# Optimization experiments

Hardware: AMD Instinct MI355X
Metric: run time of the kernel (lower is better)

The kernel has to match this reference:

```python
import jax, jax.numpy as jnp
import numpy as np

N, E, H, D, IN = 50000, 800000, 4, 16, 64  # nodes, edges, heads, head dim, in_feats
HD = H * D


def setup_inputs() -> dict:
    key = jax.random.key(0)
    ks = jax.random.split(key, 12)
    inp = {
        "q_src": jax.random.normal(ks[0], (N, H, D), jnp.float32),
        "v_src": jax.random.normal(ks[1], (N, H, D), jnp.float32),
        "feat": jax.random.normal(ks[2], (N, IN), jnp.float32),
        "src": jax.random.randint(ks[3], (E,), 0, N, jnp.int32),
        "dst": jax.random.randint(ks[4], (E,), 0, N, jnp.int32),
        # parameters (torch nn.Linear stores W as [out, in]; we use [in, out])
        "Wk": jax.random.normal(ks[5], (IN, HD), jnp.float32) / np.sqrt(IN),
        "bk": jnp.zeros((HD,), jnp.float32),
        "Wskip": jax.random.normal(ks[6], (IN, HD), jnp.float32) / np.sqrt(IN),
        "bskip": jnp.zeros((HD,), jnp.float32),
        "Wgate": jax.random.normal(ks[7], (3 * HD, 1), jnp.float32) / np.sqrt(3 * HD),
        "bgate": jnp.zeros((1,), jnp.float32),
        "ln_gamma": jnp.ones((HD,), jnp.float32),
        "ln_beta": jnp.zeros((HD,), jnp.float32),
        "prelu_a": jnp.array(0.25, jnp.float32),  # nn.PReLU() default
    }
    return inp


def reference(q_src, v_src, feat, src, dst, Wk, bk, Wskip, bskip, Wgate, bgate, ln_gamma, ln_beta, prelu_a):
    n = feat.shape[0]
    # k_dst = lin_key(h_dst).view(-1, H, D)
    k_dst = (feat @ Wk + bk).reshape(n, H, D)
    # per-edge dot-product scores: u_dot_v('ft','ft') -> [E, H, 1], scaled
    a = jnp.sum(q_src[src] * k_dst[dst], axis=-1, keepdims=True) / np.sqrt(D)
    # edge softmax over incoming edges of each dst node (segment softmax)
    amax = jax.lax.stop_gradient(jax.ops.segment_max(a, dst, num_segments=n))  # [n,H,1]
    ex = jnp.exp(a - amax[dst])
    denom = jax.ops.segment_sum(ex, dst, num_segments=n)  # [n,H,1]
    sa = ex / denom[dst]  # [E,H,1]
    # u_mul_e + sum: weighted scatter-sum aggregation
    agg = jax.ops.segment_sum(v_src[src] * sa, dst, num_segments=n)  # [n,H,D]
    rst = agg.reshape(n, HD)
    # skip connection + gate
    skip = feat @ Wskip + bskip  # [n, HD]
    gate = jax.nn.sigmoid(jnp.concatenate([skip, rst, skip - rst], axis=-1) @ Wgate + bgate)
    rst = gate * skip + (1.0 - gate) * rst
    # LayerNorm over last dim (eps=1e-5)
    mu = jnp.mean(rst, axis=-1, keepdims=True)
    var = jnp.mean(jnp.square(rst - mu), axis=-1, keepdims=True)
    rst = (rst - mu) * jax.lax.rsqrt(var + 1e-5) * ln_gamma + ln_beta
    # PReLU activation
    rst = jnp.where(rst >= 0, rst, prelu_a * rst)
    return rst
```

## Files before the change

kernel.cpp:

```cpp
#include <hip/hip_runtime.h>
#include <hip/hip_fp16.h>

#define NN 50000
#define EE 800000
#define MAXDEG 64
#define NBUCK 98
#define BSHIFT 9
#define BMASK 511
#define CAP 9216
#define AB_BLOCKS 1564

typedef _Float16 f16x8 __attribute__((ext_vector_type(8)));
typedef float    f32x4 __attribute__((ext_vector_type(4)));

union F4H { float4 f4; __half2 h2[4]; };

__global__ void zero_kernel(int* __restrict__ gcursor)
{
    if (threadIdx.x < NBUCK) gcursor[threadIdx.x] = 0;
}

__global__ __launch_bounds__(256) void binpack_kernel(
    const float* __restrict__ feat,
    const float* __restrict__ Wk, const float* __restrict__ bk,
    const float* __restrict__ Ws, const float* __restrict__ bs,
    const float* __restrict__ q, const float* __restrict__ v,
    const int* __restrict__ src, const int* __restrict__ dst,
    __half2* __restrict__ ks,
    __half2* __restrict__ qv, int* __restrict__ gcursor,
    int* __restrict__ staging)
{
    __shared__ f16x8 sFrag[16 * 64];
    __shared__ int hist[NBUCK], gbase[NBUCK];

    int tid = threadIdx.x, bid = blockIdx.x;

    if ((bid & 1) == 0) {
        if (tid < NBUCK) hist[tid] = 0;
        __syncthreads();

        int ebid  = bid >> 1;
        int ebase = ebid * 1024 + tid * 4;
        int4 es, ed;
        int b0 = 0, b1 = 0, b2 = 0, b3 = 0, r0 = 0, r1 = 0, r2 = 0, r3 = 0;
        bool ev = ebase < EE;
        if (ev) {
            es = *(const int4*)(src + ebase);
            ed = *(const int4*)(dst + ebase);
            b0 = ed.x >> BSHIFT; r0 = atomicAdd(&hist[b0], 1);
            b1 = ed.y >> BSHIFT; r1 = atomicAdd(&hist[b1], 1);
            b2 = ed.z >> BSHIFT; r2 = atomicAdd(&hist[b2], 1);
            b3 = ed.w >> BSHIFT; r3 = atomicAdd(&hist[b3], 1);
        }
        __syncthreads();
        if (tid < NBUCK) {
            int h = hist[tid];
            gbase[tid] = h ? atomicAdd(gcursor + tid, h) : 0;
        }
        __syncthreads();
        if (ev) {
            int i0 = gbase[b0] + r0; if (i0 < CAP) staging[b0 * CAP + i0] = (es.x << BSHIFT) | (ed.x & BMASK);
            int i1 = gbase[b1] + r1; if (i1 < CAP) staging[b1 * CAP + i1] = (es.y << BSHIFT) | (ed.y & BMASK);
            int i2 = gbase[b2] + r2; if (i2 < CAP) staging[b2 * CAP + i2] = (es.z << BSHIFT) | (ed.z & BMASK);
            int i3 = gbase[b3] + r3; if (i3 < CAP) staging[b3 * CAP + i3] = (es.w << BSHIFT) | (ed.w & BMASK);
        }
        return;
    }

    int nbid = bid >> 1;
    int wave = tid >> 6, lane = tid & 63;

    for (int i = tid; i < 4096; i += 256) {
        int k = i >> 6, nk = i & 63;
        int kt = k >> 5, j = k & 7;
        int lf = ((k >> 3) & 3) * 16 + (nk & 15);
        ((_Float16*)&sFrag[((nk >> 4) * 2 + kt) * 64 + lf])[j]       = (_Float16)Wk[i];
        ((_Float16*)&sFrag[((4 + (nk >> 4)) * 2 + kt) * 64 + lf])[j] = (_Float16)Ws[i];
    }
    __syncthreads();

    int base16 = nbid * 64 + wave * 16;
    if (base16 < NN) {
        int m  = lane & 15;
        int kg = lane >> 4;
        const float* arow = feat + (size_t)(base16 + m) * 64 + kg * 8;
        float4 fa0 = *(const float4*)(arow + 0);
        float4 fa1 = *(const float4*)(arow + 4);
        float4 fa2 = *(const float4*)(arow + 32);
        float4 fa3 = *(const float4*)(arow + 36);
        f16x8 a0 = { (_Float16)fa0.x,(_Float16)fa0.y,(_Float16)fa0.z,(_Float16)fa0.w,
                     (_Float16)fa1.x,(_Float16)fa1.y,(_Float16)fa1.z,(_Float16)fa1.w };
        f16x8 a1 = { (_Float16)fa2.x,(_Float16)fa2.y,(_Float16)fa2.z,(_Float16)fa2.w,
                     (_Float16)fa3.x,(_Float16)fa3.y,(_Float16)fa3.z,(_Float16)fa3.w };

        f32x4 acc0={0,0,0,0}, acc1={0,0,0,0}, acc2={0,0,0,0}, acc3={0,0,0,0};
        f32x4 acc4={0,0,0,0}, acc5={0,0,0,0}, acc6={0,0,0,0}, acc7={0,0,0,0};

#define COLT(c, ACC) { \
        f16x8 b0 = sFrag[((c)*2 + 0) * 64 + lane]; \
        f16x8 b1 = sFrag[((c)*2 + 1) * 64 + lane]; \
        ACC = __builtin_amdgcn_mfma_f32_16x16x32_f16(a0, b0, ACC, 0, 0, 0); \
        ACC = __builtin_amdgcn_mfma_f32_16x16x32_f16(a1, b1, ACC, 0, 0, 0); }
        COLT(0, acc0) COLT(1, acc1) COLT(2, acc2) COLT(3, acc3)
        COLT(4, acc4) COLT(5, acc5) COLT(6, acc6) COLT(7, acc7)
#undef COLT

        int rbase = base16 + kg * 4;

#define STOREP(COFF, AK, AS) { \
        int col = (COFF) + m; float bbk = bk[col], bbs = bs[col]; \
        ks[(size_t)(rbase + 0) * 64 + col] = __floats2half2_rn(AK[0] + bbk, AS[0] + bbs); \
        ks[(size_t)(rbase + 1) * 64 + col] = __floats2half2_rn(AK[1] + bbk, AS[1] + bbs); \
        ks[(size_t)(rbase + 2) * 64 + col] = __floats2half2_rn(AK[2] + bbk, AS[2] + bbs); \
        ks[(size_t)(rbase + 3) * 64 + col] = __floats2half2_rn(AK[3] + bbk, AS[3] + bbs); }
        STOREP( 0, acc0, acc4) STOREP(16, acc1, acc5)
        STOREP(32, acc2, acc6) STOREP(48, acc3, acc7)
#undef STOREP
    }

    {
        size_t g0 = (size_t)nbid * 4096 + (size_t)tid * 16;
        if ((int)(g0 >> 6) < NN) {
            const float4* qp = (const float4*)(q + g0);
            const float4* vp = (const float4*)(v + g0);
            #pragma unroll
            for (int gI = 0; gI < 4; ++gI) {
                float4 qq = qp[gI], vv = vp[gI];
                F4H outw;
                outw.h2[0] = __floats2half2_rn(qq.x, vv.x);
                outw.h2[1] = __floats2half2_rn(qq.y, vv.y);
                outw.h2[2] = __floats2half2_rn(qq.z, vv.z);
                outw.h2[3] = __floats2half2_rn(qq.w, vv.w);
                *(float4*)(qv + g0 + gI * 4) = outw.f4;
            }
        }
    }
}

__global__ __launch_bounds__(256) void scatter_kernel(
    const int* __restrict__ staging, const int* __restrict__ gcursor,
    unsigned short* __restrict__ sorted_src,
    int* __restrict__ cntA, int* __restrict__ cntB)
{
    __shared__ int cnt[512];
    int b = blockIdx.x >> 1, half = blockIdx.x & 1, tid = threadIdx.x;
    cnt[tid] = 0; cnt[tid + 256] = 0;
    __syncthreads();

    int nE = gcursor[b];
    if (nE > CAP) nE = CAP;
    int lo = half ? (nE >> 1) : 0;
    int hi = half ? nE : (nE >> 1);

    if (half == 0) {
        for (int i = lo + tid; i < hi; i += 256) {
            int e  = staging[b * CAP + i];
            int dl = e & BMASK;
            int pos = atomicAdd(&cnt[dl], 1);
            if (pos < MAXDEG)
                sorted_src[(size_t)((b << BSHIFT) + dl) * MAXDEG + pos] =
                    (unsigned short)(e >> BSHIFT);
        }
    } else {
        for (int i = lo + tid; i < hi; i += 256) {
            int e  = staging[b * CAP + i];
            int dl = e & BMASK;
            int pos = atomicAdd(&cnt[dl], 1);
            int sl = MAXDEG - 1 - pos;
            if (sl >= 0)
                sorted_src[(size_t)((b << BSHIFT) + dl) * MAXDEG + sl] =
                    (unsigned short)(e >> BSHIFT);
        }
    }
    __syncthreads();

    int* cp = half ? cntB : cntA;
    int d0 = (b << BSHIFT) + tid;
    if (d0 < NN) cp[d0] = cnt[tid];
    int d1 = d0 + 256;
    if (d1 < NN) cp[d1] = cnt[tid + 256];
}

__global__ __launch_bounds__(256) void gather_finalize_kernel(
    const __half2* __restrict__ qv,
    const __half2* __restrict__ ks,
    const unsigned short* __restrict__ sorted_src,
    const int*     __restrict__ cntA,
    const int*     __restrict__ cntB,
    const float*   __restrict__ Wg,
    const float*   __restrict__ bg,
    const float*   __restrict__ gamma,
    const float*   __restrict__ beta,
    const float*   __restrict__ prelu_a,
    float* __restrict__ out, int n)
{
    int node = (blockIdx.x * 256 + threadIdx.x) >> 6;
    int lane = threadIdx.x & 63;
    if (node >= n) return;
    int g = lane >> 4;
    int w = lane & 15;
    int slot = w * 4;

    int cA = cntA[node];
    int dcount = cA + cntB[node];
    if (dcount > MAXDEG) dcount = MAXDEG;
    int sidx = (lane < cA) ? lane : (MAXDEG - 1 - (lane - cA));
    int s_all = (lane < dcount) ? (int)sorted_src[(size_t)node * MAXDEG + sidx] : 0;

    F4H ksr;
    ksr.f4 = *(const float4*)(ks + (size_t)node * 64 + slot);
    float2 ks0 = __half22float2(ksr.h2[0]);
    float2 ks1 = __half22float2(ksr.h2[1]);
    float2 ks2 = __half22float2(ksr.h2[2]);
    float2 ks3 = __half22float2(ksr.h2[3]);
    float4 k4;  k4.x = ks0.x;  k4.y = ks1.x;  k4.z = ks2.x;  k4.w = ks3.x;
    float4 sk4; sk4.x = ks0.y; sk4.y = ks1.y; sk4.z = ks2.y; sk4.w = ks3.y;

    float wg0a = Wg[slot],      wg1a = Wg[slot+1],      wg2a = Wg[slot+2],      wg3a = Wg[slot+3];
    float wg0b = Wg[64+slot],   wg1b = Wg[64+slot+1],   wg2b = Wg[64+slot+2],   wg3b = Wg[64+slot+3];
    float wg0c = Wg[128+slot],  wg1c = Wg[128+slot+1],  wg2c = Wg[128+slot+2],  wg3c = Wg[128+slot+3];
    float gm0 = gamma[slot], gm1 = gamma[slot+1], gm2 = gamma[slot+2], gm3 = gamma[slot+3];
    float bt0 = beta[slot],  bt1 = beta[slot+1],  bt2 = beta[slot+2],  bt3 = beta[slot+3];
    float bgv = bg[0];
    float al  = prelu_a[0];

    float den = 0.f;
    float acc0 = 0.f, acc1 = 0.f, acc2 = 0.f, acc3 = 0.f;

    int niter = (dcount + 7) >> 3;
    if (niter > 0) {
        int sA = __shfl(s_all, g);
        int sB = __shfl(s_all, 4 + g);
        F4H rA, rB;
        rA.f4 = *(const float4*)(qv + (size_t)sA * 64 + slot);
        rB.f4 = *(const float4*)(qv + (size_t)sB * 64 + slot);

        for (int it = 0; it < niter; ++it) {
            F4H cAx = rA, cBx = rB;
            int e0 = it * 8;
            if (it + 1 < niter) {
                int sA2 = __shfl(s_all, (e0 + 8 + g) & 63);
                int sB2 = __shfl(s_all, (e0 + 12 + g) & 63);
                rA.f4 = *(const float4*)(qv + (size_t)sA2 * 64 + slot);
                rB.f4 = *(const float4*)(qv + (size_t)sB2 * 64 + slot);
            }

            {
                float2 a0 = __half22float2(cAx.h2[0]);
                float2 a1 = __half22float2(cAx.h2[1]);
                float2 a2 = __half22float2(cAx.h2[2]);
                float2 a3 = __half22float2(cAx.h2[3]);
                float p = a0.x * k4.x + a1.x * k4.y + a2.x * k4.z + a3.x * k4.w;
                p += __shfl_xor(p, 1);
                p += __shfl_xor(p, 2);
                float ex = ((e0 + g) < dcount) ? __expf(p * 0.25f) : 0.f;
                den += ex;
                acc0 = fmaf(ex, a0.y, acc0);
                acc1 = fmaf(ex, a1.y, acc1);
                acc2 = fmaf(ex, a2.y, acc2);
                acc3 = fmaf(ex, a3.y, acc3);
            }

            if (e0 + 4 < dcount) {
                float2 b0 = __half22float2(cBx.h2[0]);
                float2 b1 = __half22float2(cBx.h2[1]);
                float2 b2 = __half22float2(cBx.h2[2]);
                float2 b3 = __half22float2(cBx.h2[3]);
                float p = b0.x * k4.x + b1.x * k4.y + b2.x * k4.z + b3.x * k4.w;
                p += __shfl_xor(p, 1);
                p += __shfl_xor(p, 2);
                float ex = ((e0 + 4 + g) < dcount) ? __expf(p * 0.25f) : 0.f;
                den += ex;
                acc0 = fmaf(ex, b0.y, acc0);
                acc1 = fmaf(ex, b1.y, acc1);
                acc2 = fmaf(ex, b2.y, acc2);
                acc3 = fmaf(ex, b3.y, acc3);
            }
        }
    }

    den  += __shfl_xor(den, 16);  den  += __shfl_xor(den, 32);
    acc0 += __shfl_xor(acc0, 16); acc0 += __shfl_xor(acc0, 32);
    acc1 += __shfl_xor(acc1, 16); acc1 += __shfl_xor(acc1, 32);
    acc2 += __shfl_xor(acc2, 16); acc2 += __shfl_xor(acc2, 32);
    acc3 += __shfl_xor(acc3, 16); acc3 += __shfl_xor(acc3, 32);

    float inv = (den > 0.f) ? 1.f / den : 0.f;
    float r0 = acc0 * inv, r1 = acc1 * inv, r2 = acc2 * inv, r3 = acc3 * inv;

    float gp = sk4.x * wg0a + r0 * wg0b + (sk4.x - r0) * wg0c
             + sk4.y * wg1a + r1 * wg1b + (sk4.y - r1) * wg1c
             + sk4.z * wg2a + r2 * wg2b + (sk4.z - r2) * wg2c
             + sk4.w * wg3a + r3 * wg3b + (sk4.w - r3) * wg3c;
    gp += __shfl_xor(gp, 1);
    gp += __shfl_xor(gp, 2);
    gp += __shfl_xor(gp, 4);
    gp += __shfl_xor(gp, 8);
    float gate = 1.f / (1.f + __expf(-(gp + bgv)));

    float m0 = gate * sk4.x + (1.f - gate) * r0;
    float m1 = gate * sk4.y + (1.f - gate) * r1;
    float m2 = gate * sk4.z + (1.f - gate) * r2;
    float m3 = gate * sk4.w + (1.f - gate) * r3;

    float mu = m0 + m1 + m2 + m3;
    mu += __shfl_xor(mu, 1); mu += __shfl_xor(mu, 2);
    mu += __shfl_xor(mu, 4); mu += __shfl_xor(mu, 8);
    mu *= (1.f / 64.f);
    float d0 = m0 - mu, d1 = m1 - mu, d2 = m2 - mu, d3 = m3 - mu;
    float var = d0 * d0 + d1 * d1 + d2 * d2 + d3 * d3;
    var += __shfl_xor(var, 1); var += __shfl_xor(var, 2);
    var += __shfl_xor(var, 4); var += __shfl_xor(var, 8);
    var *= (1.f / 64.f);
    float rs = rsqrtf(var + 1e-5f);

    float y0 = d0 * rs * gm0 + bt0;
    float y1 = d1 * rs * gm1 + bt1;
    float y2 = d2 * rs * gm2 + bt2;
    float y3 = d3 * rs * gm3 + bt3;
    y0 = (y0 >= 0.f) ? y0 : al * y0;
    y1 = (y1 >= 0.f) ? y1 : al * y1;
    y2 = (y2 >= 0.f) ? y2 : al * y2;
    y3 = (y3 >= 0.f) ? y3 : al * y3;

    if (g == 0) {
        float4 o; o.x = y0; o.y = y1; o.z = y2; o.w = y3;
        *(float4*)(out + (size_t)node * 64 + slot) = o;
    }
}

extern "C" void kernel_launch(void* const* d_in, const int* in_sizes, int n_in,
                              void* d_out, int out_size, void* d_ws, size_t ws_size,
                              hipStream_t stream)
{
    const float* q_src  = (const float*)d_in[0];
    const float* v_src  = (const float*)d_in[1];
    const float* feat   = (const float*)d_in[2];
    const int*   src    = (const int*)d_in[3];
    const int*   dst    = (const int*)d_in[4];
    const float* Wk     = (const float*)d_in[5];
    const float* bk     = (const float*)d_in[6];
    const float* Wskip  = (const float*)d_in[7];
    const float* bskip  = (const float*)d_in[8];
    const float* Wgate  = (const float*)d_in[9];
    const float* bgate  = (const float*)d_in[10];
    const float* ln_g   = (const float*)d_in[11];
    const float* ln_b   = (const float*)d_in[12];
    const float* prelu  = (const float*)d_in[13];

    float* out = (float*)d_out;

    char* ws = (char*)d_ws;
    const size_t A = (size_t)NN * 64 * 4;
    __half2*        ks         = (__half2*)(ws);
    __half2*        qv         = (__half2*)(ws + A);
    unsigned short* sorted_src = (unsigned short*)(ws + 2 * A);
    size_t off = 2 * A + A / 2;
    int* cntA    = (int*)(ws + off);            off += (size_t)NN * 4;
    int* cntB    = (int*)(ws + off);            off += (size_t)NN * 4;
    int* gcursor = (int*)(ws + off);            off += 4096;
    int* staging = (int*)(ws + off);

    zero_kernel<<<1, 128, 0, stream>>>(gcursor);

    binpack_kernel<<<AB_BLOCKS, 256, 0, stream>>>(
        feat, Wk, bk, Wskip, bskip, q_src, v_src, src, dst,
        ks, qv, gcursor, staging);

    scatter_kernel<<<NBUCK * 2, 256, 0, stream>>>(staging, gcursor,
                                                  sorted_src, cntA, cntB);

    int gblk = (NN * 64 + 255) / 256;
    gather_finalize_kernel<<<gblk, 256, 0, stream>>>(qv, ks,
                                                     sorted_src, cntA, cntB,
                                                     Wgate, bgate, ln_g, ln_b,
                                                     prelu, out, NN);
}
```

Measured before the change: 79.27 us.

## Split q/v fp16 layout, use fdot2 for scores, per-wave LDS histograms

Changes the packed q/v buffer from interleaved half2 pairs to a per-node row holding q halves then v halves. The gather loads q and v as separate 8-byte chunks and computes the score with packed fp16 dot2 instructions instead of converting to fp32. The binning pass also gives each wave its own LDS histogram to reduce atomic contention, with per-wave offsets taken from one global atomic. The intent is fewer conversion ALU ops and less LDS contention, at the cost of two gather loads per edge instead of one and fp16-accumulated dot products.

```diff
diff --git a/kernel.cpp b/kernel.cpp
--- a/kernel.cpp
+++ b/kernel.cpp
@@ -9,11 +9,25 @@
 #define BMASK 511
 #define CAP 9216
 #define AB_BLOCKS 1564
+#define HPAD 104
 
 typedef _Float16 f16x8 __attribute__((ext_vector_type(8)));
+typedef _Float16 h8   __attribute__((ext_vector_type(8)));
+typedef _Float16 h2v  __attribute__((ext_vector_type(2)));
 typedef float    f32x4 __attribute__((ext_vector_type(4)));
 
 union F4H { float4 f4; __half2 h2[4]; };
+union H4  { float2 f2; h2v h2[2]; };
+
+__device__ __forceinline__ float qdot4(h2v q01, h2v q23, h2v k01, h2v k23) {
+#if __has_builtin(__builtin_amdgcn_fdot2)
+    return __builtin_amdgcn_fdot2(q01, k01,
+           __builtin_amdgcn_fdot2(q23, k23, 0.f, false), false);
+#else
+    return (float)q01[0] * (float)k01[0] + (float)q01[1] * (float)k01[1]
+         + (float)q23[0] * (float)k23[0] + (float)q23[1] * (float)k23[1];
+#endif
+}
 
 __global__ void zero_kernel(int* __restrict__ gcursor)
 {
@@ -27,16 +41,18 @@
     const float* __restrict__ q, const float* __restrict__ v,
     const int* __restrict__ src, const int* __restrict__ dst,
     __half2* __restrict__ ks,
-    __half2* __restrict__ qv, int* __restrict__ gcursor,
+    _Float16* __restrict__ qvh,
+    int* __restrict__ gcursor,
     int* __restrict__ staging)
 {
     __shared__ f16x8 sFrag[16 * 64];
-    __shared__ int hist[NBUCK], gbase[NBUCK];
+    __shared__ int hist[4][HPAD], gbase[4][HPAD];
 
     int tid = threadIdx.x, bid = blockIdx.x;
+    int wave = tid >> 6, lane = tid & 63;
 
     if ((bid & 1) == 0) {
-        if (tid < NBUCK) hist[tid] = 0;
+        for (int i = tid; i < 4 * HPAD; i += 256) hist[i / HPAD][i % HPAD] = 0;
         __syncthreads();
 
         int ebid  = bid >> 1;
@@ -47,28 +63,33 @@
         if (ev) {
             es = *(const int4*)(src + ebase);
             ed = *(const int4*)(dst + ebase);
-            b0 = ed.x >> BSHIFT; r0 = atomicAdd(&hist[b0], 1);
-            b1 = ed.y >> BSHIFT; r1 = atomicAdd(&hist[b1], 1);
-            b2 = ed.z >> BSHIFT; r2 = atomicAdd(&hist[b2], 1);
-            b3 = ed.w >> BSHIFT; r3 = atomicAdd(&hist[b3], 1);
+            b0 = ed.x >> BSHIFT; r0 = atomicAdd(&hist[wave][b0], 1);
+            b1 = ed.y >> BSHIFT; r1 = atomicAdd(&hist[wave][b1], 1);
+            b2 = ed.z >> BSHIFT; r2 = atomicAdd(&hist[wave][b2], 1);
+            b3 = ed.w >> BSHIFT; r3 = atomicAdd(&hist[wave][b3], 1);
         }
         __syncthreads();
         if (tid < NBUCK) {
-            int h = hist[tid];
-            gbase[tid] = h ? atomicAdd(gcursor + tid, h) : 0;
+            int h0 = hist[0][tid], h1 = hist[1][tid];
+            int h2 = hist[2][tid], h3 = hist[3][tid];
+            int tot = h0 + h1 + h2 + h3;
+            int base = tot ? atomicAdd(gcursor + tid, tot) : 0;
+            gbase[0][tid] = base;
+            gbase[1][tid] = base + h0;
+            gbase[2][tid] = base + h0 + h1;
+            gbase[3][tid] = base + h0 + h1 + h2;
         }
         __syncthreads();
         if (ev) {
-            int i0 = gbase[b0] + r0; if (i0 < CAP) staging[b0 * CAP + i0] = (es.x << BSHIFT) | (ed.x & BMASK);
-            int i1 = gbase[b1] + r1; if (i1 < CAP) staging[b1 * CAP + i1] = (es.y << BSHIFT) | (ed.y & BMASK);
-            int i2 = gbase[b2] + r2; if (i2 < CAP) staging[b2 * CAP + i2] = (es.z << BSHIFT) | (ed.z & BMASK);
-            int i3 = gbase[b3] + r3; if (i3 < CAP) staging[b3 * CAP + i3] = (es.w << BSHIFT) | (ed.w & BMASK);
+            int i0 = gbase[wave][b0] + r0; if (i0 < CAP) staging[b0 * CAP + i0] = (es.x << BSHIFT) | (ed.x & BMASK);
+            int i1 = gbase[wave][b1] + r1; if (i1 < CAP) staging[b1 * CAP + i1] = (es.y << BSHIFT) | (ed.y & BMASK);
+            int i2 = gbase[wave][b2] + r2; if (i2 < CAP) staging[b2 * CAP + i2] = (es.z << BSHIFT) | (ed.z & BMASK);
+            int i3 = gbase[wave][b3] + r3; if (i3 < CAP) staging[b3 * CAP + i3] = (es.w << BSHIFT) | (ed.w & BMASK);
         }
         return;
     }
 
     int nbid = bid >> 1;
-    int wave = tid >> 6, lane = tid & 63;
 
     for (int i = tid; i < 4096; i += 256) {
         int k = i >> 6, nk = i & 63;
@@ -120,19 +141,26 @@
 
     {
         size_t g0 = (size_t)nbid * 4096 + (size_t)tid * 16;
-        if ((int)(g0 >> 6) < NN) {
+        int node = (int)(g0 >> 6);
+        int col0 = (int)(g0 & 63);
+        if (node < NN) {
             const float4* qp = (const float4*)(q + g0);
             const float4* vp = (const float4*)(v + g0);
-            #pragma unroll
-            for (int gI = 0; gI < 4; ++gI) {
-                float4 qq = qp[gI], vv = vp[gI];
-                F4H outw;
-                outw.h2[0] = __floats2half2_rn(qq.x, vv.x);
-                outw.h2[1] = __floats2half2_rn(qq.y, vv.y);
-                outw.h2[2] = __floats2half2_rn(qq.z, vv.z);
-                outw.h2[3] = __floats2half2_rn(qq.w, vv.w);
-                *(float4*)(qv + g0 + gI * 4) = outw.f4;
-            }
+            float4 q0 = qp[0], q1 = qp[1], q2 = qp[2], q3 = qp[3];
+            float4 v0 = vp[0], v1 = vp[1], v2 = vp[2], v3 = vp[3];
+            h8 qa = { (_Float16)q0.x,(_Float16)q0.y,(_Float16)q0.z,(_Float16)q0.w,
+                      (_Float16)q1.x,(_Float16)q1.y,(_Float16)q1.z,(_Float16)q1.w };
+            h8 qb = { (_Float16)q2.x,(_Float16)q2.y,(_Float16)q2.z,(_Float16)q2.w,
+                      (_Float16)q3.x,(_Float16)q3.y,(_Float16)q3.z,(_Float16)q3.w };
+            h8 va = { (_Float16)v0.x,(_Float16)v0.y,(_Float16)v0.z,(_Float16)v0.w,
+                      (_Float16)v1.x,(_Float16)v1.y,(_Float16)v1.z,(_Float16)v1.w };
+            h8 vb = { (_Float16)v2.x,(_Float16)v2.y,(_Float16)v2.z,(_Float16)v2.w,
+                      (_Float16)v3.x,(_Float16)v3.y,(_Float16)v3.z,(_Float16)v3.w };
+            _Float16* row = qvh + (size_t)node * 128;
+            *(h8*)(row + col0)          = qa;
+            *(h8*)(row + col0 + 8)      = qb;
+            *(h8*)(row + 64 + col0)     = va;
+            *(h8*)(row + 64 + col0 + 8) = vb;
         }
     }
 }
@@ -182,8 +210,8 @@
 }
 
 __global__ __launch_bounds__(256) void gather_finalize_kernel(
-    const __half2* __restrict__ qv,
-    const __half2* __restrict__ ks,
+    const _Float16* __restrict__ qvh,
+    const __half2*  __restrict__ ks,
     const unsigned short* __restrict__ sorted_src,
     const int*     __restrict__ cntA,
     const int*     __restrict__ cntB,
@@ -213,8 +241,9 @@
     float2 ks1 = __half22float2(ksr.h2[1]);
     float2 ks2 = __half22float2(ksr.h2[2]);
     float2 ks3 = __half22float2(ksr.h2[3]);
-    float4 k4;  k4.x = ks0.x;  k4.y = ks1.x;  k4.z = ks2.x;  k4.w = ks3.x;
     float4 sk4; sk4.x = ks0.y; sk4.y = ks1.y; sk4.z = ks2.y; sk4.w = ks3.y;
+    h2v kh01 = { (_Float16)ks0.x, (_Float16)ks1.x };
+    h2v kh23 = { (_Float16)ks2.x, (_Float16)ks3.x };
 
     float wg0a = Wg[slot],      wg1a = Wg[slot+1],      wg2a = Wg[slot+2],      wg3a = Wg[slot+3];
     float wg0b = Wg[64+slot],   wg1b = Wg[64+slot+1],   wg2b = Wg[64+slot+2],   wg3b = Wg[64+slot+3];
@@ -231,50 +260,46 @@
     if (niter > 0) {
         int sA = __shfl(s_all, g);
         int sB = __shfl(s_all, 4 + g);
-        F4H rA, rB;
-        rA.f4 = *(const float4*)(qv + (size_t)sA * 64 + slot);
-        rB.f4 = *(const float4*)(qv + (size_t)sB * 64 + slot);
+        H4 qA, vA, qB, vB;
+        qA.f2 = *(const float2*)(qvh + (size_t)sA * 128 + slot);
+        vA.f2 = *(const float2*)(qvh + (size_t)sA * 128 + 64 + slot);
+        qB.f2 = *(const float2*)(qvh + (size_t)sB * 128 + slot);
+        vB.f2 = *(const float2*)(qvh + (size_t)sB * 128 + 64 + slot);
 
         for (int it = 0; it < niter; ++it) {
-            F4H cAx = rA, cBx = rB;
+            H4 cqA = qA, cvA = vA, cqB = qB, cvB = vB;
             int e0 = it * 8;
             if (it + 1 < niter) {
                 int sA2 = __shfl(s_all, (e0 + 8 + g) & 63);
                 int sB2 = __shfl(s_all, (e0 + 12 + g) & 63);
-                rA.f4 = *(const float4*)(qv + (size_t)sA2 * 64 + slot);
-                rB.f4 = *(const float4*)(qv + (size_t)sB2 * 64 + slot);
+                qA.f2 = *(const float2*)(qvh + (size_t)sA2 * 128 + slot);
+                vA.f2 = *(const float2*)(qvh + (size_t)sA2 * 128 + 64 + slot);
+                qB.f2 = *(const float2*)(qvh + (size_t)sB2 * 128 + slot);
+                vB.f2 = *(const float2*)(qvh + (size_t)sB2 * 128 + 64 + slot);
             }
 
             {
-                float2 a0 = __half22float2(cAx.h2[0]);
-                float2 a1 = __half22float2(cAx.h2[1]);
-                float2 a2 = __half22float2(cAx.h2[2]);
-                float2 a3 = __half22float2(cAx.h2[3]);
-                float p = a0.x * k4.x + a1.x * k4.y + a2.x * k4.z + a3.x * k4.w;
+                float p = qdot4(cqA.h2[0], cqA.h2[1], kh01, kh23);
                 p += __shfl_xor(p, 1);
                 p += __shfl_xor(p, 2);
                 float ex = ((e0 + g) < dcount) ? __expf(p * 0.25f) : 0.f;
                 den += ex;
-                acc0 = fmaf(ex, a0.y, acc0);
-                acc1 = fmaf(ex, a1.y, acc1);
-                acc2 = fmaf(ex, a2.y, acc2);
-                acc3 = fmaf(ex, a3.y, acc3);
+                acc0 = fmaf(ex, (float)cvA.h2[0][0], acc0);
+                acc1 = fmaf(ex, (float)cvA.h2[0][1], acc1);
+                acc2 = fmaf(ex, (float)cvA.h2[1][0], acc2);
+                acc3 = fmaf(ex, (float)cvA.h2[1][1], acc3);
             }
 
             if (e0 + 4 < dcount) {
-                float2 b0 = __half22float2(cBx.h2[0]);
-                float2 b1 = __half22float2(cBx.h2[1]);
-                float2 b2 = __half22float2(cBx.h2[2]);
-                float2 b3 = __half22float2(cBx.h2[3]);
-                float p = b0.x * k4.x + b1.x * k4.y + b2.x * k4.z + b3.x * k4.w;
+                float p = qdot4(cqB.h2[0], cqB.h2[1], kh01, kh23);
                 p += __shfl_xor(p, 1);
                 p += __shfl_xor(p, 2);
                 float ex = ((e0 + 4 + g) < dcount) ? __expf(p * 0.25f) : 0.f;
                 den += ex;
-                acc0 = fmaf(ex, b0.y, acc0);
-                acc1 = fmaf(ex, b1.y, acc1);
-                acc2 = fmaf(ex, b2.y, acc2);
-                acc3 = fmaf(ex, b3.y, acc3);
+                acc0 = fmaf(ex, (float)cvB.h2[0][0], acc0);
+                acc1 = fmaf(ex, (float)cvB.h2[0][1], acc1);
+                acc2 = fmaf(ex, (float)cvB.h2[1][0], acc2);
+                acc3 = fmaf(ex, (float)cvB.h2[1][1], acc3);
             }
         }
     }
@@ -353,7 +378,7 @@
     char* ws = (char*)d_ws;
     const size_t A = (size_t)NN * 64 * 4;
     __half2*        ks         = (__half2*)(ws);
-    __half2*        qv         = (__half2*)(ws + A);
+    _Float16*       qvh        = (_Float16*)(ws + A);
     unsigned short* sorted_src = (unsigned short*)(ws + 2 * A);
     size_t off = 2 * A + A / 2;
     int* cntA    = (int*)(ws + off);            off += (size_t)NN * 4;
@@ -365,13 +390,13 @@
 
     binpack_kernel<<<AB_BLOCKS, 256, 0, stream>>>(
         feat, Wk, bk, Wskip, bskip, q_src, v_src, src, dst,
-        ks, qv, gcursor, staging);
+        ks, qvh, gcursor, staging);
 
     scatter_kernel<<<NBUCK * 2, 256, 0, stream>>>(staging, gcursor,
                                                   sorted_src, cntA, cntB);
 
     int gblk = (NN * 64 + 255) / 256;
-    gather_finalize_kernel<<<gblk, 256, 0, stream>>>(qv, ks,
+    gather_finalize_kernel<<<gblk, 256, 0, stream>>>(qvh, ks,
                                                      sorted_src, cntA, cntB,
                                                      Wgate, bgate, ln_g, ln_b,
                                                      prelu, out, NN);
```

Result: no change. 79.07 us (-0.3%).
